# Optimization experiments

Hardware: AMD Instinct MI355X
Metric: run time of the kernel (lower is better)

Reference implementation:

```python
import jax, jax.numpy as jnp
import numpy as np

N_RAYS = 65536   # 256x256 image
N_PTS = 128      # samples per ray
FEAT = 3         # RGB
FAR_DELTA = 1e10 # sentinel delta for last sample, as in the torch module


def setup_inputs() -> dict:
    key = jax.random.key(0)
    k1, k2, k3 = jax.random.split(key, 3)
    # depths along each ray must be increasing (deltas computed by diff)
    depth_values = jnp.sort(
        jax.random.uniform(k1, (N_RAYS, N_PTS), jnp.float32, 2.0, 6.0), axis=-1)
    density = jax.random.uniform(k2, (N_RAYS, N_PTS), jnp.float32)  # non-negative
    feature = jax.random.uniform(k3, (N_RAYS, N_PTS, FEAT), jnp.float32)
    return {"depth_values": depth_values, "density": density, "feature": feature}


def reference(depth_values, density, feature):
    n_rays, n_pts = depth_values.shape
    # deltas: consecutive depth differences, huge value appended for last bin
    deltas = jnp.concatenate(
        [depth_values[:, 1:] - depth_values[:, :-1],
         jnp.full((n_rays, 1), FAR_DELTA, depth_values.dtype)], axis=-1)
    tau = density * deltas                              # [n_rays, n_pts]
    # transmittance T_i = exp(-sum_{j<i} tau_j) (exclusive cumsum in log space)
    log_T = -jnp.concatenate(
        [jnp.zeros((n_rays, 1), tau.dtype), jnp.cumsum(tau[:, :-1], axis=-1)],
        axis=-1)
    weights = jnp.exp(log_T) * (1.0 - jnp.exp(-tau))    # [n_rays, n_pts]
    feat_out = jnp.einsum('np,npf->nf', weights, feature)         # [n_rays, F]
    depth_out = jnp.sum(weights * depth_values, axis=-1, keepdims=True)
    return jnp.concatenate([feat_out, depth_out], axis=-1)        # [n_rays, F+1]
```

## Files before the change

### kernel.cpp

```cpp
#include <hip/hip_runtime.h>

#define N_RAYS 65536
#define N_PTS  128
#define FAR_DELTA 1e10f

#define BLOCK   256
#define NBLOCKS 1024
#define NWAVES  (NBLOCKS * (BLOCK / 64))
#define NPAIRS  (N_RAYS / 2)
#define NP      (NPAIRS / NWAVES)

#define ROW_SHR(n)  (0x110 | (n))
#define ROW_SHL(n)  (0x100 | (n))
#define ROW_BCAST15 0x142

template<int CTRL, int RMASK, bool BC>
__device__ __forceinline__ float dpp_f(float x) {
    return __builtin_bit_cast(float,
        __builtin_amdgcn_update_dpp(0, __builtin_bit_cast(int, x),
                                    CTRL, RMASK, 0xF, BC));
}

__global__ __launch_bounds__(BLOCK) void volrend_kernel(
    const float* __restrict__ depth,
    const float* __restrict__ density,
    const float* __restrict__ feature,
    float* __restrict__ out)
{
    __shared__ float4 sbuf[4][2][5 * 64];

    const int tid  = threadIdx.x;
    const int w    = tid >> 6;
    const int lane = tid & 63;
    const int sl   = lane & 31;
    const int g    = (int)blockIdx.x * (BLOCK / 64) + w;

#define GLD(gp_, lp_)                                                         \
    __builtin_amdgcn_global_load_lds(                                         \
        (const __attribute__((address_space(1))) void*)(gp_),                 \
        (__attribute__((address_space(3))) void*)(lp_), 16, 0, 0)

#define ISSUE(p_, b_)                                                         \
    do {                                                                      \
        float4* wb_ = &sbuf[w][b_][0];                                        \
        GLD(depth   + (size_t)(p_) * 256 + 4 * lane, wb_);                    \
        GLD(density + (size_t)(p_) * 256 + 4 * lane, wb_ + 64);               \
        const float* fp_ = feature + (size_t)(p_) * 768 + 4 * lane;           \
        GLD(fp_,       wb_ + 128);                                            \
        GLD(fp_ + 256, wb_ + 192);                                            \
        GLD(fp_ + 512, wb_ + 256);                                            \
    } while (0)

    ISSUE(g, 0);
    ISSUE(NWAVES + g, 1);

#pragma unroll
    for (int p = 0; p < NP; ++p) {
        if      (p == 0)      asm volatile("s_waitcnt vmcnt(5)" ::: "memory");
        else if (p == 1)      asm volatile("s_waitcnt vmcnt(6)" ::: "memory");
        else if (p < NP - 1)  asm volatile("s_waitcnt vmcnt(7)" ::: "memory");
        else                  asm volatile("s_waitcnt vmcnt(2)" ::: "memory");

        const float4* wb   = &sbuf[w][p & 1][0];
        const float*  ldsf = (const float*)wb;
        float4 d   = wb[lane];
        float4 rho = wb[64 + lane];
        float4 f0  = wb[128 + 3 * lane];
        float4 f1  = wb[129 + 3 * lane];
        float4 f2  = wb[130 + 3 * lane];
        float  nx  = ldsf[4 * lane + 4];

        asm volatile("s_waitcnt lgkmcnt(0)" ::: "memory");
        if (p + 2 < NP) ISSUE((p + 2) * NWAVES + g, p & 1);

        float t0 = rho.x * (d.y - d.x);
        float t1 = rho.y * (d.z - d.y);
        float t2 = rho.z * (d.w - d.z);
        float t3 = rho.w * ((sl == 31) ? FAR_DELTA : (nx - d.w));
        float q1 = t0, q2 = q1 + t1, q3 = q2 + t2, tot = q3 + t3;

        float incl = tot;
        incl += dpp_f<ROW_SHR(1), 0xF, true>(incl);
        incl += dpp_f<ROW_SHR(2), 0xF, true>(incl);
        incl += dpp_f<ROW_SHR(4), 0xF, true>(incl);
        incl += dpp_f<ROW_SHR(8), 0xF, true>(incl);
        float e = dpp_f<ROW_SHR(1), 0xF, true>(incl);
        e += dpp_f<ROW_BCAST15, 0xA, false>(incl);

        float T0 = __expf(-e);
        float T1 = __expf(-(e + q1));
        float T2 = __expf(-(e + q2));
        float T3 = __expf(-(e + q3));
        float T4 = __expf(-(e + tot));
        float w0 = T0 - T1, w1 = T1 - T2, w2 = T2 - T3, w3 = T3 - T4;

        float a3 = w0 * d.x  + w1 * d.y  + w2 * d.z  + w3 * d.w;
        float a0 = w0 * f0.x + w1 * f0.w + w2 * f1.z + w3 * f2.y;
        float a1 = w0 * f0.y + w1 * f1.x + w2 * f1.w + w3 * f2.z;
        float a2 = w0 * f0.z + w1 * f1.y + w2 * f2.x + w3 * f2.w;

#define RED(a_)                                                               \
    do {                                                                      \
        a_ += dpp_f<ROW_SHL(8), 0xF, true>(a_);                               \
        a_ += dpp_f<ROW_SHL(4), 0xF, true>(a_);                               \
        a_ += dpp_f<ROW_SHL(2), 0xF, true>(a_);                               \
        a_ += dpp_f<ROW_SHL(1), 0xF, true>(a_);                               \
        a_ += __builtin_bit_cast(float,                                       \
            __builtin_amdgcn_ds_swizzle(__builtin_bit_cast(int, a_), 0x401F));\
    } while (0)
        RED(a0); RED(a1); RED(a2); RED(a3);
#undef RED

        if (sl == 0) {
            int ray = 2 * (p * NWAVES + g) + (lane >> 5);
            *(float4*)(out + (size_t)ray * 4) = make_float4(a0, a1, a2, a3);
        }
    }
#undef ISSUE
#undef GLD
}

extern "C" void kernel_launch(void* const* d_in, const int* in_sizes, int n_in,
                              void* d_out, int out_size, void* d_ws, size_t ws_size,
                              hipStream_t stream) {
    const float* depth   = (const float*)d_in[0];
    const float* density = (const float*)d_in[1];
    const float* feature = (const float*)d_in[2];
    float* out = (float*)d_out;

    dim3 grid(NBLOCKS);
    dim3 block(BLOCK);
    volrend_kernel<<<grid, block, 0, stream>>>(depth, density, feature, out);
}
```

Measured before the change: 194.6 us.

## Load ray data directly into registers with register double-buffering, double block count

Drops the LDS staging path (global_load_lds into shared buffers followed by LDS reads). Each lane now loads its depth, density, next-depth and its 12 contiguous feature floats straight into VGPRs with inline-asm global loads. The next ray pair is prefetched into a second register set. The grid doubles to 2048 blocks, which halves iterations per wave and raises the number of waves in flight to hide memory latency. The risk is that the inline-asm loads are invisible to the compiler's wait tracking, so correctness relies on the hand-placed vmcnt waits and on the end-of-loop register copies being eliminated or ordered safely.

```diff
diff --git a/kernel.cpp b/kernel.cpp
--- a/kernel.cpp
+++ b/kernel.cpp
@@ -5,10 +5,12 @@
 #define FAR_DELTA 1e10f
 
 #define BLOCK   256
-#define NBLOCKS 1024
+#define NBLOCKS 2048
 #define NWAVES  (NBLOCKS * (BLOCK / 64))
 #define NPAIRS  (N_RAYS / 2)
 #define NP      (NPAIRS / NWAVES)
+
+typedef float f32x4 __attribute__((ext_vector_type(4)));
 
 #define ROW_SHR(n)  (0x110 | (n))
 #define ROW_SHL(n)  (0x100 | (n))
@@ -27,51 +29,41 @@
     const float* __restrict__ feature,
     float* __restrict__ out)
 {
-    __shared__ float4 sbuf[4][2][5 * 64];
+    const int lane = threadIdx.x & 63;
+    const int sl   = lane & 31;
+    const int g    = (int)blockIdx.x * (BLOCK / 64) + (threadIdx.x >> 6);
 
-    const int tid  = threadIdx.x;
-    const int w    = tid >> 6;
-    const int lane = tid & 63;
-    const int sl   = lane & 31;
-    const int g    = (int)blockIdx.x * (BLOCK / 64) + w;
+    f32x4 d, rho, f0, f1, f2;  float nx;
+    f32x4 pd, pr, pf0, pf1, pf2; float pnx;
 
-#define GLD(gp_, lp_)                                                         \
-    __builtin_amdgcn_global_load_lds(                                         \
-        (const __attribute__((address_space(1))) void*)(gp_),                 \
-        (__attribute__((address_space(3))) void*)(lp_), 16, 0, 0)
+#define GLD4(dst_, gp_) \
+    asm volatile("global_load_dwordx4 %0, %1, off" : "=v"(dst_) : "v"(gp_))
+#define GLD1(dst_, gp_) \
+    asm volatile("global_load_dword %0, %1, off"   : "=v"(dst_) : "v"(gp_))
 
-#define ISSUE(p_, b_)                                                         \
+#define ISSUE(p_, D_, R_, F0_, F1_, F2_, NX_)                                 \
     do {                                                                      \
-        float4* wb_ = &sbuf[w][b_][0];                                        \
-        GLD(depth   + (size_t)(p_) * 256 + 4 * lane, wb_);                    \
-        GLD(density + (size_t)(p_) * 256 + 4 * lane, wb_ + 64);               \
-        const float* fp_ = feature + (size_t)(p_) * 768 + 4 * lane;           \
-        GLD(fp_,       wb_ + 128);                                            \
-        GLD(fp_ + 256, wb_ + 192);                                            \
-        GLD(fp_ + 512, wb_ + 256);                                            \
+        const float* dp_ = depth + (size_t)(p_) * 256 + 4 * lane;             \
+        GLD4(D_, dp_);                                                        \
+        GLD1(NX_, dp_ + ((sl == 31) ? 3 : 4));                                \
+        GLD4(R_, density + (size_t)(p_) * 256 + 4 * lane);                    \
+        const float* fp_ = feature + (size_t)(p_) * 768 + 12 * lane;          \
+        GLD4(F0_, fp_);                                                       \
+        GLD4(F1_, fp_ + 4);                                                   \
+        GLD4(F2_, fp_ + 8);                                                   \
     } while (0)
 
-    ISSUE(g, 0);
-    ISSUE(NWAVES + g, 1);
+    ISSUE(g, d, rho, f0, f1, f2, nx);
 
 #pragma unroll
     for (int p = 0; p < NP; ++p) {
-        if      (p == 0)      asm volatile("s_waitcnt vmcnt(5)" ::: "memory");
-        else if (p == 1)      asm volatile("s_waitcnt vmcnt(6)" ::: "memory");
-        else if (p < NP - 1)  asm volatile("s_waitcnt vmcnt(7)" ::: "memory");
-        else                  asm volatile("s_waitcnt vmcnt(2)" ::: "memory");
+        if (p + 1 < NP)
+            ISSUE((p + 1) * NWAVES + g, pd, pr, pf0, pf1, pf2, pnx);
 
-        const float4* wb   = &sbuf[w][p & 1][0];
-        const float*  ldsf = (const float*)wb;
-        float4 d   = wb[lane];
-        float4 rho = wb[64 + lane];
-        float4 f0  = wb[128 + 3 * lane];
-        float4 f1  = wb[129 + 3 * lane];
-        float4 f2  = wb[130 + 3 * lane];
-        float  nx  = ldsf[4 * lane + 4];
-
-        asm volatile("s_waitcnt lgkmcnt(0)" ::: "memory");
-        if (p + 2 < NP) ISSUE((p + 2) * NWAVES + g, p & 1);
+        if      (p == 0)      asm volatile("s_waitcnt vmcnt(6)" ::: "memory");
+        else if (p <  NP - 1) asm volatile("s_waitcnt vmcnt(7)" ::: "memory");
+        else                  asm volatile("s_waitcnt vmcnt(1)" ::: "memory");
+        __builtin_amdgcn_sched_barrier(0);
 
         float t0 = rho.x * (d.y - d.x);
         float t1 = rho.y * (d.z - d.y);
@@ -115,9 +107,12 @@
             int ray = 2 * (p * NWAVES + g) + (lane >> 5);
             *(float4*)(out + (size_t)ray * 4) = make_float4(a0, a1, a2, a3);
         }
+
+        d = pd; rho = pr; f0 = pf0; f1 = pf1; f2 = pf2; nx = pnx;
     }
 #undef ISSUE
-#undef GLD
+#undef GLD4
+#undef GLD1
 }
 
 extern "C" void kernel_launch(void* const* d_in, const int* in_sizes, int n_in,
```

Result: no change. 196.6 us (+1.0%).
